# Kernel tuning notes

Measured on AMD Instinct MI355X. Metric: run time of the kernel, lower is better.

Reference implementation:

```python
import jax, jax.numpy as jnp
import numpy as np

MLP_CHANNELS = 128
MLP_KERNEL = 5


def setup_inputs() -> dict:
    key = jax.random.key(0)
    k1, k2 = jax.random.split(key)
    b, c, h, w = 16, MLP_CHANNELS, 128, 128
    num_w = MLP_KERNEL ** 2 * c + c  # 3328
    inp = jax.random.normal(k1, (b, c, h, w), dtype=jnp.float32)
    # mimic ini_weights_ scaling: conv weights ~ N(0, 6/(k^2+c)), bias ~ N(0, 1/c)
    weights = jax.random.normal(k2, (b, num_w), dtype=jnp.float32)
    off = MLP_KERNEL ** 2 * c
    scale = jnp.concatenate([
        jnp.full((off,), np.sqrt(6.0 / (MLP_KERNEL ** 2 + c)), dtype=jnp.float32),
        jnp.full((c,), np.sqrt(1.0 / c), dtype=jnp.float32),
    ])
    weights = weights * scale[None, :]
    return {"input": inp, "weights": weights}


def reference(input, weights):
    b, c, h, w = input.shape
    k = MLP_KERNEL
    off = k * k * c
    # per-sample depthwise filters [b, c, 1, k, k] and biases [b, c]
    wk = weights[:, :off].reshape(b, c, 1, k, k)
    bias = weights[:, off:off + c]

    def dwconv(x, wt):
        # x: [c,h,w], wt: [c,1,k,k]; depthwise conv via feature_group_count=c
        return jax.lax.conv_general_dilated(
            x[None], wt, window_strides=(1, 1), padding='SAME',
            dimension_numbers=('NCHW', 'OIHW', 'NCHW'),
            feature_group_count=c)[0]

    out = jax.vmap(dwconv)(input, wk)          # [b,c,h,w]
    out = out + bias[:, :, None, None]          # fused bias
    return jax.nn.silu(out)                     # act
```

## Files before the change

### kernel.cpp

```cpp
#include <hip/hip_runtime.h>
#include <math.h>

#define C_CH 128
#define HW 128
#define KK 5
#define PAD 2
#define TILE_ROWS 64
#define LDS_ROWS (TILE_ROWS + 2*PAD)
#define LDS_COLS (HW + 2*PAD)
#define NW (KK*KK*C_CH + C_CH)

__global__ __launch_bounds__(256, 4) void hyperconv_dw_silu(
    const float* __restrict__ inp, const float* __restrict__ wts,
    float* __restrict__ out)
{
    __shared__ float s[LDS_ROWS][LDS_COLS];

    const int tid  = threadIdx.x;
    const int tile = blockIdx.x;
    const int c    = blockIdx.y;
    const int b    = blockIdx.z;

    const float* wt = wts + (size_t)b * NW;
    float wk[25];
    #pragma unroll
    for (int j = 0; j < 25; ++j) wk[j] = wt[c * 25 + j];
    const float bias = wt[KK*KK*C_CH + c];

    const int row0 = tile * TILE_ROWS;
    const float* plane = inp + ((size_t)(b * C_CH + c)) * (HW * HW);

    for (int i = tid; i < LDS_ROWS * 4; i += 256) {
        int r  = i >> 2;
        int ci = i & 3;
        int col = (ci < 2) ? ci : (HW + ci);
        s[r][col] = 0.0f;
    }

    for (int idx = tid; idx < LDS_ROWS * (HW / 4); idx += 256) {
        int r  = idx >> 5;
        int cs = idx & 31;
        int gr = row0 - PAD + r;
        float4 v = make_float4(0.f, 0.f, 0.f, 0.f);
        if (gr >= 0 && gr < HW) {
            v = *(const float4*)(plane + (size_t)gr * HW + cs * 4);
        }
        float2* dst = (float2*)&s[r][2 + cs * 4];
        dst[0] = make_float2(v.x, v.y);
        dst[1] = make_float2(v.z, v.w);
    }
    __syncthreads();

    const int colg = tid & 31;
    const int rowg = tid >> 5;
    float* oplane = out + ((size_t)(b * C_CH + c)) * (HW * HW);

    #pragma unroll
    for (int p = 0; p < 2; ++p) {
        const int ro = p * 32 + rowg * 4;

        float acc[4][4];
        #pragma unroll
        for (int i = 0; i < 4; ++i)
            #pragma unroll
            for (int j = 0; j < 4; ++j)
                acc[i][j] = bias;

        #pragma unroll
        for (int r = 0; r < 8; ++r) {
            const float4 a  = *(const float4*)&s[ro + r][colg * 4];
            const float4 bb = *(const float4*)&s[ro + r][colg * 4 + 4];
            float x[8] = {a.x, a.y, a.z, a.w, bb.x, bb.y, bb.z, bb.w};

            #pragma unroll
            for (int orow = 0; orow < 4; ++orow) {
                const int kh = r - orow;
                if (kh < 0 || kh > 4) continue;
                #pragma unroll
                for (int oc = 0; oc < 4; ++oc) {
                    #pragma unroll
                    for (int kw = 0; kw < 5; ++kw) {
                        acc[orow][oc] = fmaf(wk[kh * 5 + kw], x[oc + kw], acc[orow][oc]);
                    }
                }
            }
        }

        #pragma unroll
        for (int orow = 0; orow < 4; ++orow) {
            float4 o;
            float v0 = acc[orow][0], v1 = acc[orow][1], v2 = acc[orow][2], v3 = acc[orow][3];
            o.x = v0 / (1.0f + expf(-v0));
            o.y = v1 / (1.0f + expf(-v1));
            o.z = v2 / (1.0f + expf(-v2));
            o.w = v3 / (1.0f + expf(-v3));
            *(float4*)(oplane + (size_t)(row0 + ro + orow) * HW + colg * 4) = o;
        }
    }
}

extern "C" void kernel_launch(void* const* d_in, const int* in_sizes, int n_in,
                              void* d_out, int out_size, void* d_ws, size_t ws_size,
                              hipStream_t stream) {
    const float* inp = (const float*)d_in[0];
    const float* wts = (const float*)d_in[1];
    float* out = (float*)d_out;

    const int batch = in_sizes[1] / NW;
    dim3 grid(HW / TILE_ROWS, C_CH, batch);
    hyperconv_dw_silu<<<grid, 256, 0, stream>>>(inp, wts, out);
}
```

Before: 239.3 us.

## Load input tiles directly to LDS via global_load_lds with smaller tiles

Each input tile is now copied straight from global memory into shared memory with the global_load_lds builtin, and the padded LDS layout is dropped. Column halos are instead handled in registers with selects, and boundary rows are zero-filled only for the edge tiles. The tile is halved to 32 rows, with occupancy hints raised so more blocks fit per CU, and SiLU uses fast exp and reciprocal intrinsics. Halving the tile raises the halo-row overhead, and the fast math intrinsics slightly reduce accuracy.

```diff
diff --git a/kernel.cpp b/kernel.cpp
--- a/kernel.cpp
+++ b/kernel.cpp
@@ -5,16 +5,17 @@
 #define HW 128
 #define KK 5
 #define PAD 2
-#define TILE_ROWS 64
+#define TILE_ROWS 32
 #define LDS_ROWS (TILE_ROWS + 2*PAD)
-#define LDS_COLS (HW + 2*PAD)
 #define NW (KK*KK*C_CH + C_CH)
+#define N_TILES (HW / TILE_ROWS)
+#define CHUNKS ((LDS_ROWS * HW * 4) / 1024)
 
-__global__ __launch_bounds__(256, 4) void hyperconv_dw_silu(
+__global__ __launch_bounds__(256, 8) void hyperconv_dw_silu(
     const float* __restrict__ inp, const float* __restrict__ wts,
     float* __restrict__ out)
 {
-    __shared__ float s[LDS_ROWS][LDS_COLS];
+    __shared__ float s[LDS_ROWS][HW];
 
     const int tid  = threadIdx.x;
     const int tile = blockIdx.x;
@@ -23,79 +24,84 @@
 
     const float* wt = wts + (size_t)b * NW;
     float wk[25];
-    #pragma unroll
+#pragma unroll
     for (int j = 0; j < 25; ++j) wk[j] = wt[c * 25 + j];
-    const float bias = wt[KK*KK*C_CH + c];
+    const float bias = wt[KK * KK * C_CH + c];
 
     const int row0 = tile * TILE_ROWS;
     const float* plane = inp + ((size_t)(b * C_CH + c)) * (HW * HW);
+    const float* src0  = plane + (row0 - PAD) * HW;
 
-    for (int i = tid; i < LDS_ROWS * 4; i += 256) {
-        int r  = i >> 2;
-        int ci = i & 3;
-        int col = (ci < 2) ? ci : (HW + ci);
-        s[r][col] = 0.0f;
+    const int wave = tid >> 6;
+    const int lane = tid & 63;
+
+    for (int ch = wave; ch < CHUNKS; ch += 4) {
+        const bool oob = (tile == 0 && ch == 0) ||
+                         (tile == N_TILES - 1 && ch == CHUNKS - 1);
+        if (!oob) {
+            __builtin_amdgcn_global_load_lds(
+                (const __attribute__((address_space(1))) void*)(src0 + ch * 256 + lane * 4),
+                (__attribute__((address_space(3))) void*)((char*)&s[0][0] + ch * 1024),
+                16, 0, 0);
+        }
     }
-
-    for (int idx = tid; idx < LDS_ROWS * (HW / 4); idx += 256) {
-        int r  = idx >> 5;
-        int cs = idx & 31;
-        int gr = row0 - PAD + r;
-        float4 v = make_float4(0.f, 0.f, 0.f, 0.f);
-        if (gr >= 0 && gr < HW) {
-            v = *(const float4*)(plane + (size_t)gr * HW + cs * 4);
-        }
-        float2* dst = (float2*)&s[r][2 + cs * 4];
-        dst[0] = make_float2(v.x, v.y);
-        dst[1] = make_float2(v.z, v.w);
-    }
+    if (tile == 0 && tid < 64)
+        *(float4*)((char*)&s[0][0] + tid * 16) = make_float4(0.f, 0.f, 0.f, 0.f);
+    if (tile == N_TILES - 1 && tid < 64)
+        *(float4*)((char*)&s[0][0] + (CHUNKS - 1) * 1024 + tid * 16) =
+            make_float4(0.f, 0.f, 0.f, 0.f);
     __syncthreads();
 
     const int colg = tid & 31;
     const int rowg = tid >> 5;
+    const int ro   = rowg * 4;
+    const int xb   = colg * 4;
+
+    const int lcb = (colg == 0)  ? 0   : (xb - 4);
+    const int rcb = (colg == 31) ? 120 : (xb + 4);
+
+    float acc[4][4];
+#pragma unroll
+    for (int i = 0; i < 4; ++i)
+#pragma unroll
+        for (int j = 0; j < 4; ++j) acc[i][j] = bias;
+
+#pragma unroll
+    for (int r = 0; r < 8; ++r) {
+        const float* srow = &s[ro + r][0];
+        const float4 xl = *(const float4*)(srow + lcb);
+        const float4 xm = *(const float4*)(srow + xb);
+        const float4 xr = *(const float4*)(srow + rcb);
+        float x[8];
+        x[0] = (colg == 0)  ? 0.f : xl.z;
+        x[1] = (colg == 0)  ? 0.f : xl.w;
+        x[2] = xm.x; x[3] = xm.y; x[4] = xm.z; x[5] = xm.w;
+        x[6] = (colg == 31) ? 0.f : xr.x;
+        x[7] = (colg == 31) ? 0.f : xr.y;
+
+#pragma unroll
+        for (int orow = 0; orow < 4; ++orow) {
+            const int kh = r - orow;
+            if (kh < 0 || kh > 4) continue;
+#pragma unroll
+            for (int oc = 0; oc < 4; ++oc)
+#pragma unroll
+                for (int kw = 0; kw < 5; ++kw)
+                    acc[orow][oc] = fmaf(wk[kh * 5 + kw], x[oc + kw], acc[orow][oc]);
+        }
+    }
+
     float* oplane = out + ((size_t)(b * C_CH + c)) * (HW * HW);
-
-    #pragma unroll
-    for (int p = 0; p < 2; ++p) {
-        const int ro = p * 32 + rowg * 4;
-
-        float acc[4][4];
-        #pragma unroll
-        for (int i = 0; i < 4; ++i)
-            #pragma unroll
-            for (int j = 0; j < 4; ++j)
-                acc[i][j] = bias;
-
-        #pragma unroll
-        for (int r = 0; r < 8; ++r) {
-            const float4 a  = *(const float4*)&s[ro + r][colg * 4];
-            const float4 bb = *(const float4*)&s[ro + r][colg * 4 + 4];
-            float x[8] = {a.x, a.y, a.z, a.w, bb.x, bb.y, bb.z, bb.w};
-
-            #pragma unroll
-            for (int orow = 0; orow < 4; ++orow) {
-                const int kh = r - orow;
-                if (kh < 0 || kh > 4) continue;
-                #pragma unroll
-                for (int oc = 0; oc < 4; ++oc) {
-                    #pragma unroll
-                    for (int kw = 0; kw < 5; ++kw) {
-                        acc[orow][oc] = fmaf(wk[kh * 5 + kw], x[oc + kw], acc[orow][oc]);
-                    }
-                }
-            }
-        }
-
-        #pragma unroll
-        for (int orow = 0; orow < 4; ++orow) {
-            float4 o;
-            float v0 = acc[orow][0], v1 = acc[orow][1], v2 = acc[orow][2], v3 = acc[orow][3];
-            o.x = v0 / (1.0f + expf(-v0));
-            o.y = v1 / (1.0f + expf(-v1));
-            o.z = v2 / (1.0f + expf(-v2));
-            o.w = v3 / (1.0f + expf(-v3));
-            *(float4*)(oplane + (size_t)(row0 + ro + orow) * HW + colg * 4) = o;
-        }
+#pragma unroll
+    for (int orow = 0; orow < 4; ++orow) {
+        float v0 = acc[orow][0], v1 = acc[orow][1];
+        float v2 = acc[orow][2], v3 = acc[orow][3];
+        float4 o;
+        o.x = v0 * __builtin_amdgcn_rcpf(1.0f + __expf(-v0));
+        o.y = v1 * __builtin_amdgcn_rcpf(1.0f + __expf(-v1));
+        o.z = v2 * __builtin_amdgcn_rcpf(1.0f + __expf(-v2));
+        o.w = v3 * __builtin_amdgcn_rcpf(1.0f + __expf(-v3));
+        *(float4*)(oplane + (size_t)(row0 + ro + orow) * HW + xb) = o;
     }
 }
 
@@ -107,6 +113,6 @@
     float* out = (float*)d_out;
 
     const int batch = in_sizes[1] / NW;
-    dim3 grid(HW / TILE_ROWS, C_CH, batch);
+    dim3 grid(N_TILES, C_CH, batch);
     hyperconv_dw_silu<<<grid, 256, 0, stream>>>(inp, wts, out);
 }
```

Measured after the change: 243.3 us. No clear change (+1.7%).
